# Performance work log

Measured on AMD Instinct MI355X. Metric: run time of the kernel, lower is better.

Reference implementation:

```python
import jax, jax.numpy as jnp
import numpy as np

ALPHA = 0.2  # LeakyReLU negative slope


def setup_inputs() -> dict:
    key = jax.random.key(0)
    k1, k2, k3, k4 = jax.random.split(key, 4)
    N, E, F_IN, F_OUT = 100000, 1600000, 128, 32
    x = jax.random.normal(k1, (N, F_IN), dtype=jnp.float32)
    W = jax.random.normal(k2, (F_IN, F_OUT), dtype=jnp.float32) * 0.1
    a = jax.random.normal(k3, (2 * F_OUT, 1), dtype=jnp.float32) * 0.1
    edge_index = jax.random.randint(k4, (2, E), 0, N, dtype=jnp.int64)
    return {"x": x, "W": W, "a": a, "edge_index": edge_index}


def reference(x, W, a, edge_index):
    N = x.shape[0]
    F_OUT = W.shape[1]
    Wx = x @ W  # [N, F_OUT]
    src = edge_index[0]  # row indices (softmax groups)
    dst = edge_index[1]
    # e = leakyrelu([Wx_i || Wx_j] @ a); split a to avoid materializing the concat
    a_src = a[:F_OUT, 0]
    a_dst = a[F_OUT:, 0]
    e = (Wx @ a_src)[src] + (Wx @ a_dst)[dst]  # [E]
    e = jnp.where(e >= 0, e, ALPHA * e)
    # sparse softmax over rows (src)
    m = jax.ops.segment_max(e, src, num_segments=N)  # -inf for empty rows
    m = jnp.where(jnp.isinf(m), 0.0, m)
    exp_v = jnp.exp(e - m[src])
    s = jax.ops.segment_sum(exp_v, src, num_segments=N)
    s = jnp.where(s == 0, 1.0, s)
    att = exp_v / s[src]  # [E]
    # sparse matmul: h[i] = sum_j att[i,j] * Wx[j]
    h = jax.ops.segment_sum(att[:, None] * Wx[dst], src, num_segments=N)
    return jax.nn.elu(h)
```

## Files before the change

### kernel.cpp

```cpp
#include <hip/hip_runtime.h>
#include <hip/hip_bf16.h>
#include <math.h>

#define ALPHA 0.2f
#define F_IN 128
#define F_OUT 32
#define BSHIFT 7
#define BNODES 128
#define DSTBITS 17
#define CHUNK 8192
#define SLABCAP 3072
#define NBKMAX 800
#define MAXPER 6
#define CURSTRIDE 16

typedef __attribute__((ext_vector_type(8))) short short8;
typedef __attribute__((ext_vector_type(4))) float float4v;

__device__ __forceinline__ short f2bf(float f) {
    __hip_bfloat16 h = __float2bfloat16(f);
    return __builtin_bit_cast(short, h);
}
__device__ __forceinline__ float bf_lo(unsigned u) {
    return __uint_as_float(u << 16);
}
__device__ __forceinline__ float bf_hi(unsigned u) {
    return __uint_as_float(u & 0xFFFF0000u);
}

__global__ __launch_bounds__(512) void k_phaseA(
    const float* __restrict__ x, const float* __restrict__ W,
    const float* __restrict__ a, unsigned short* __restrict__ Wxh,
    float* __restrict__ s1, float* __restrict__ s2, int nTiles, int N, int nT1,
    const int* __restrict__ src, const int* __restrict__ dst,
    int* __restrict__ bcur, unsigned* __restrict__ packed, int E, int NBK)
{
    if ((int)blockIdx.x < nT1) {
        __shared__ short Wt[32 * 136];
        for (int i = threadIdx.x; i < F_IN * F_OUT; i += 512) {
            int k = i >> 5, n = i & 31;
            Wt[n * 136 + k] = f2bf(W[i]);
        }
        __syncthreads();

        int wave = threadIdx.x >> 6;
        int lane = threadIdx.x & 63;
        int tile = blockIdx.x * 8 + wave;
        if (tile >= nTiles) return;

        int m    = lane & 15;
        int quad = lane >> 4;
        int row  = tile * 16 + m;
        int rowc = row < N ? row : N - 1;

        short8 bf[2][4];
#pragma unroll
        for (int t = 0; t < 2; ++t)
#pragma unroll
            for (int s = 0; s < 4; ++s)
                bf[t][s] = *(const short8*)&Wt[(t * 16 + m) * 136 + s * 32 + quad * 8];

        float4v acc0 = {0.f, 0.f, 0.f, 0.f};
        float4v acc1 = {0.f, 0.f, 0.f, 0.f};
        const float* xr = x + (size_t)rowc * F_IN + quad * 8;
#pragma unroll
        for (int s = 0; s < 4; ++s) {
            float4 xa = *(const float4*)(xr + s * 32);
            float4 xb = *(const float4*)(xr + s * 32 + 4);
            short8 af;
            af[0] = f2bf(xa.x); af[1] = f2bf(xa.y); af[2] = f2bf(xa.z); af[3] = f2bf(xa.w);
            af[4] = f2bf(xb.x); af[5] = f2bf(xb.y); af[6] = f2bf(xb.z); af[7] = f2bf(xb.w);
            acc0 = __builtin_amdgcn_mfma_f32_16x16x32_bf16(af, bf[0][s], acc0, 0, 0, 0);
            acc1 = __builtin_amdgcn_mfma_f32_16x16x32_bf16(af, bf[1][s], acc1, 0, 0, 0);
        }

        int rbase = tile * 16 + quad * 4;
#pragma unroll
        for (int r = 0; r < 4; ++r) {
            if (rbase + r < N) {
                Wxh[(size_t)(rbase + r) * F_OUT + m]      = (unsigned short)f2bf(acc0[r]);
                Wxh[(size_t)(rbase + r) * F_OUT + m + 16] = (unsigned short)f2bf(acc1[r]);
            }
        }

        float a1c0 = a[m], a1c1 = a[m + 16];
        float a2c0 = a[F_OUT + m], a2c1 = a[F_OUT + m + 16];
#pragma unroll
        for (int r = 0; r < 4; ++r) {
            float v1 = acc0[r] * a1c0 + acc1[r] * a1c1;
            float v2 = acc0[r] * a2c0 + acc1[r] * a2c1;
#pragma unroll
            for (int off = 8; off >= 1; off >>= 1) {
                v1 += __shfl_xor(v1, off, 16);
                v2 += __shfl_xor(v2, off, 16);
            }
            if (m == 0 && rbase + r < N) {
                s1[rbase + r] = v1;
                s2[rbase + r] = v2;
            }
        }
    } else {
        __shared__ int hist[NBKMAX];
        __shared__ int cur[NBKMAX];
        int t = threadIdx.x;
        for (int i = t; i < NBK; i += 512) hist[i] = 0;
        __syncthreads();
        int e0 = ((int)blockIdx.x - nT1) * CHUNK;
        int sreg[16], dreg[16];
#pragma unroll
        for (int k = 0; k < 4; ++k) {
            int e = e0 + k * 2048 + t * 4;
            int4 s4, d4;
            if (e + 3 < E) {
                s4 = *(const int4*)&src[e];
                d4 = *(const int4*)&dst[e];
            } else {
                s4.x = (e + 0 < E) ? src[e + 0] : -1;
                s4.y = (e + 1 < E) ? src[e + 1] : -1;
                s4.z = (e + 2 < E) ? src[e + 2] : -1;
                s4.w = (e + 3 < E) ? src[e + 3] : -1;
                d4.x = (e + 0 < E) ? dst[e + 0] : 0;
                d4.y = (e + 1 < E) ? dst[e + 1] : 0;
                d4.z = (e + 2 < E) ? dst[e + 2] : 0;
                d4.w = (e + 3 < E) ? dst[e + 3] : 0;
            }
            sreg[k * 4 + 0] = s4.x; dreg[k * 4 + 0] = d4.x;
            sreg[k * 4 + 1] = s4.y; dreg[k * 4 + 1] = d4.y;
            sreg[k * 4 + 2] = s4.z; dreg[k * 4 + 2] = d4.z;
            sreg[k * 4 + 3] = s4.w; dreg[k * 4 + 3] = d4.w;
        }
#pragma unroll
        for (int k = 0; k < 16; ++k)
            if (sreg[k] >= 0) atomicAdd(&hist[sreg[k] >> BSHIFT], 1);
        __syncthreads();
        for (int i = t; i < NBK; i += 512)
            if (hist[i] > 0) cur[i] = atomicAdd(&bcur[i * CURSTRIDE], hist[i]);
        __syncthreads();
#pragma unroll
        for (int k = 0; k < 16; ++k) {
            if (sreg[k] >= 0) {
                int b = sreg[k] >> BSHIFT;
                int p = atomicAdd(&cur[b], 1);
                if (p < SLABCAP)
                    packed[(size_t)b * SLABCAP + p] =
                        ((unsigned)(sreg[k] & (BNODES - 1)) << DSTBITS) | (unsigned)dreg[k];
            }
        }
    }
}

__global__ __launch_bounds__(512) void k_bnode(
    const unsigned* __restrict__ packed, const int* __restrict__ bcur,
    const float* __restrict__ s1, const float* __restrict__ s2,
    const unsigned short* __restrict__ Wxh, float* __restrict__ out, int N)
{
    __shared__ unsigned sorted[SLABCAP];
    __shared__ int rpl[BNODES];
    __shared__ int degl[BNODES];
    __shared__ int cur[BNODES];
    __shared__ int histl[BNODES];
    __shared__ float s1l[BNODES];
    __shared__ float stageL[16][8][32];
    __shared__ float sumsL[16][8];

    int b = blockIdx.x;
    int t = threadIdx.x;
    int n0 = b << BSHIFT;
    int cnt = min(bcur[b * CURSTRIDE], SLABCAP);
    const unsigned* pb = packed + (size_t)b * SLABCAP;

    if (t < BNODES) {
        histl[t] = 0;
        int n = n0 + t;
        s1l[t] = (n < N) ? s1[n] : 0.f;
    }
    __syncthreads();

    unsigned ereg[MAXPER];
#pragma unroll
    for (int k = 0; k < MAXPER; ++k) {
        int j = k * 512 + t;
        ereg[k] = (j < cnt) ? pb[j] : 0xFFFFFFFFu;
    }
#pragma unroll
    for (int k = 0; k < MAXPER; ++k)
        if (ereg[k] != 0xFFFFFFFFu) atomicAdd(&histl[ereg[k] >> DSTBITS], 1);
    __syncthreads();

    if (t < 64) {
        int aLo = histl[t], aHi = histl[t + 64];
        int sLo = aLo, sHi = aHi;
#pragma unroll
        for (int off = 1; off < 64; off <<= 1) {
            int vLo = __shfl_up(sLo, off, 64);
            int vHi = __shfl_up(sHi, off, 64);
            if (t >= off) { sLo += vLo; sHi += vHi; }
        }
        sHi += __shfl(sLo, 63, 64);
        rpl[t]      = sLo - aLo;  cur[t]      = sLo - aLo;  degl[t]      = aLo;
        rpl[t + 64] = sHi - aHi;  cur[t + 64] = sHi - aHi;  degl[t + 64] = aHi;
    }
    __syncthreads();

#pragma unroll
    for (int k = 0; k < MAXPER; ++k) {
        if (ereg[k] != 0xFFFFFFFFu) {
            int ls = ereg[k] >> DSTBITS;
            int p = atomicAdd(&cur[ls], 1);
            sorted[p] = ereg[k];
        }
    }
    __syncthreads();

    int g = t >> 5;
    int l = t & 31;
    int es = l >> 3;
    int fq = l & 7;

    for (int ni = 0; ni < 8; ++ni) {
        int ls = (g << 3) + ni;
        int n = n0 + ls;
        if (n >= N) break;
        int base = rpl[ls];
        int deg  = degl[ls];
        float s1n = s1l[ls];

        float acc[4];
#pragma unroll
        for (int c = 0; c < 4; ++c) acc[c] = 0.f;
        float sum = 0.f;

        for (int j0 = 0; j0 < deg; j0 += 32) {
            int j = j0 + l;
            int   d_l = 0;
            float p_l = 0.f;
            if (j < deg) {
                d_l = (int)(sorted[base + j] & ((1u << DSTBITS) - 1));
                float ev = s1n + s2[d_l];
                ev = ev >= 0.f ? ev : ALPHA * ev;
                p_l = __expf(ev);
            }
            sum += p_l;
            int cnt2 = min(32, deg - j0);
            int nIter = (cnt2 + 3) >> 2;
            for (int it = 0; it < nIter; ++it) {
                int e = (it << 2) + es;
                float p = __shfl(p_l, e, 32);
                int   d = __shfl(d_l, e, 32);
                uint2 w = *(const uint2*)&Wxh[(size_t)d * F_OUT + fq * 4];
                acc[0] += p * bf_lo(w.x);
                acc[1] += p * bf_hi(w.x);
                acc[2] += p * bf_lo(w.y);
                acc[3] += p * bf_hi(w.y);
            }
        }
#pragma unroll
        for (int off = 8; off <= 16; off <<= 1)
#pragma unroll
            for (int c = 0; c < 4; ++c)
                acc[c] += __shfl_xor(acc[c], off, 32);
#pragma unroll
        for (int off = 16; off >= 1; off >>= 1)
            sum += __shfl_xor(sum, off, 32);

        if (l < 8) {
            float4 v;
            v.x = acc[0]; v.y = acc[1]; v.z = acc[2]; v.w = acc[3];
            *(float4*)&stageL[g][ni][l * 4] = v;
        }
        if (l == 0)
            sumsL[g][ni] = sum;
    }

    {
        int ln = l >> 2;
        int fo = (l & 3) * 8;
        int n = n0 + (g << 3) + ln;
        if (n < N) {
            float s = sumsL[g][ln];
            float inv = (s > 0.f) ? __builtin_amdgcn_rcpf(s) : 0.f;
            const float* sp = &stageL[g][ln][fo];
            float4 h0 = *(const float4*)sp;
            float4 h1 = *(const float4*)(sp + 4);
            h0.x *= inv; h0.y *= inv; h0.z *= inv; h0.w *= inv;
            h1.x *= inv; h1.y *= inv; h1.z *= inv; h1.w *= inv;
            h0.x = h0.x > 0.f ? h0.x : __expf(h0.x) - 1.f;
            h0.y = h0.y > 0.f ? h0.y : __expf(h0.y) - 1.f;
            h0.z = h0.z > 0.f ? h0.z : __expf(h0.z) - 1.f;
            h0.w = h0.w > 0.f ? h0.w : __expf(h0.w) - 1.f;
            h1.x = h1.x > 0.f ? h1.x : __expf(h1.x) - 1.f;
            h1.y = h1.y > 0.f ? h1.y : __expf(h1.y) - 1.f;
            h1.z = h1.z > 0.f ? h1.z : __expf(h1.z) - 1.f;
            h1.w = h1.w > 0.f ? h1.w : __expf(h1.w) - 1.f;
            float* op = &out[(size_t)n * F_OUT + fo];
            *(float4*)op       = h0;
            *(float4*)(op + 4) = h1;
        }
    }
}

extern "C" void kernel_launch(void* const* d_in, const int* in_sizes, int n_in,
                              void* d_out, int out_size, void* d_ws, size_t ws_size,
                              hipStream_t stream)
{
    const float* x = (const float*)d_in[0];
    const float* W = (const float*)d_in[1];
    const float* a = (const float*)d_in[2];
    const int*  ei = (const int*)d_in[3];

    int N = in_sizes[0] / F_IN;
    int E = in_sizes[3] / 2;
    const int* src = ei;
    const int* dst = ei + E;
    int NBK = (N + BNODES - 1) >> BSHIFT;
    int nTiles = (N + 15) / 16;
    int nT1 = (nTiles + 7) / 8;
    int nEB = (E + CHUNK - 1) / CHUNK;

    unsigned short* Wxh = (unsigned short*)d_ws;
    float*    s1       = (float*)d_ws + (size_t)16 * N;
    float*    s2       = s1 + N;
    int*      bcur     = (int*)(s2 + N);
    unsigned* packed   = (unsigned*)(bcur + NBKMAX * CURSTRIDE);

    float* out = (float*)d_out;

    hipMemsetAsync(bcur, 0, (size_t)NBKMAX * CURSTRIDE * 4, stream);

    k_phaseA<<<nT1 + nEB, 512, 0, stream>>>(x, W, a, Wxh, s1, s2, nTiles, N, nT1,
                                            src, dst, bcur, packed, E, NBK);
    k_bnode<<<NBK, 512, 0, stream>>>(packed, bcur, s1, s2, Wxh, out, N);
}
```

Baseline: 149.1 us.

## Fuse both phases into one cooperative persistent kernel with grid sync

Replaces the memset plus two kernel launches with a single cooperative kernel. It zeroes the counters itself, runs phase A (GEMM tiles and edge bucketing) and the per-bucket aggregation as persistent loops driven by atomic work counters, and separates the two phases with grid.sync(). Shared memory for the phases is overlaid in a union. This removes launch gaps and the memset, at the cost of grid-sync overhead, an extra atomic fetch per work item, and an occupancy limit on grid size.

```diff
diff --git a/kernel.cpp b/kernel.cpp
--- a/kernel.cpp
+++ b/kernel.cpp
@@ -1,6 +1,9 @@
 #include <hip/hip_runtime.h>
+#include <hip/hip_cooperative_groups.h>
 #include <hip/hip_bf16.h>
 #include <math.h>
+
+namespace cg = cooperative_groups;
 
 #define ALPHA 0.2f
 #define F_IN 128
@@ -28,273 +31,302 @@
     return __uint_as_float(u & 0xFFFF0000u);
 }
 
-__global__ __launch_bounds__(512) void k_phaseA(
+struct SmemGemm { short Wt[32 * 136]; };
+struct SmemBkt  { int hist[NBKMAX]; int cur[NBKMAX]; };
+struct SmemNode {
+    unsigned sorted[SLABCAP];
+    int rpl[BNODES]; int degl[BNODES]; int cur[BNODES]; int histl[BNODES];
+    float s1l[BNODES];
+    float stage[16][8][32];
+    float sums[16][8];
+};
+union SmemU { SmemGemm g; SmemBkt b; SmemNode n; };
+
+__global__ __launch_bounds__(512) void k_fused(
     const float* __restrict__ x, const float* __restrict__ W,
     const float* __restrict__ a, unsigned short* __restrict__ Wxh,
     float* __restrict__ s1, float* __restrict__ s2, int nTiles, int N, int nT1,
     const int* __restrict__ src, const int* __restrict__ dst,
-    int* __restrict__ bcur, unsigned* __restrict__ packed, int E, int NBK)
+    int* __restrict__ bcur, unsigned* __restrict__ packed, int E, int NBK,
+    int nWorkA, float* __restrict__ out)
 {
-    if ((int)blockIdx.x < nT1) {
-        __shared__ short Wt[32 * 136];
-        for (int i = threadIdx.x; i < F_IN * F_OUT; i += 512) {
-            int k = i >> 5, n = i & 31;
-            Wt[n * 136 + k] = f2bf(W[i]);
-        }
-        __syncthreads();
-
-        int wave = threadIdx.x >> 6;
-        int lane = threadIdx.x & 63;
-        int tile = blockIdx.x * 8 + wave;
-        if (tile >= nTiles) return;
-
-        int m    = lane & 15;
-        int quad = lane >> 4;
-        int row  = tile * 16 + m;
-        int rowc = row < N ? row : N - 1;
-
-        short8 bf[2][4];
-#pragma unroll
-        for (int t = 0; t < 2; ++t)
-#pragma unroll
-            for (int s = 0; s < 4; ++s)
-                bf[t][s] = *(const short8*)&Wt[(t * 16 + m) * 136 + s * 32 + quad * 8];
-
-        float4v acc0 = {0.f, 0.f, 0.f, 0.f};
-        float4v acc1 = {0.f, 0.f, 0.f, 0.f};
-        const float* xr = x + (size_t)rowc * F_IN + quad * 8;
-#pragma unroll
-        for (int s = 0; s < 4; ++s) {
-            float4 xa = *(const float4*)(xr + s * 32);
-            float4 xb = *(const float4*)(xr + s * 32 + 4);
-            short8 af;
-            af[0] = f2bf(xa.x); af[1] = f2bf(xa.y); af[2] = f2bf(xa.z); af[3] = f2bf(xa.w);
-            af[4] = f2bf(xb.x); af[5] = f2bf(xb.y); af[6] = f2bf(xb.z); af[7] = f2bf(xb.w);
-            acc0 = __builtin_amdgcn_mfma_f32_16x16x32_bf16(af, bf[0][s], acc0, 0, 0, 0);
-            acc1 = __builtin_amdgcn_mfma_f32_16x16x32_bf16(af, bf[1][s], acc1, 0, 0, 0);
-        }
-
-        int rbase = tile * 16 + quad * 4;
-#pragma unroll
-        for (int r = 0; r < 4; ++r) {
-            if (rbase + r < N) {
-                Wxh[(size_t)(rbase + r) * F_OUT + m]      = (unsigned short)f2bf(acc0[r]);
-                Wxh[(size_t)(rbase + r) * F_OUT + m + 16] = (unsigned short)f2bf(acc1[r]);
-            }
-        }
-
-        float a1c0 = a[m], a1c1 = a[m + 16];
-        float a2c0 = a[F_OUT + m], a2c1 = a[F_OUT + m + 16];
-#pragma unroll
-        for (int r = 0; r < 4; ++r) {
-            float v1 = acc0[r] * a1c0 + acc1[r] * a1c1;
-            float v2 = acc0[r] * a2c0 + acc1[r] * a2c1;
-#pragma unroll
-            for (int off = 8; off >= 1; off >>= 1) {
-                v1 += __shfl_xor(v1, off, 16);
-                v2 += __shfl_xor(v2, off, 16);
-            }
-            if (m == 0 && rbase + r < N) {
-                s1[rbase + r] = v1;
-                s2[rbase + r] = v2;
-            }
-        }
-    } else {
-        __shared__ int hist[NBKMAX];
-        __shared__ int cur[NBKMAX];
-        int t = threadIdx.x;
-        for (int i = t; i < NBK; i += 512) hist[i] = 0;
-        __syncthreads();
-        int e0 = ((int)blockIdx.x - nT1) * CHUNK;
-        int sreg[16], dreg[16];
-#pragma unroll
-        for (int k = 0; k < 4; ++k) {
-            int e = e0 + k * 2048 + t * 4;
-            int4 s4, d4;
-            if (e + 3 < E) {
-                s4 = *(const int4*)&src[e];
-                d4 = *(const int4*)&dst[e];
-            } else {
-                s4.x = (e + 0 < E) ? src[e + 0] : -1;
-                s4.y = (e + 1 < E) ? src[e + 1] : -1;
-                s4.z = (e + 2 < E) ? src[e + 2] : -1;
-                s4.w = (e + 3 < E) ? src[e + 3] : -1;
-                d4.x = (e + 0 < E) ? dst[e + 0] : 0;
-                d4.y = (e + 1 < E) ? dst[e + 1] : 0;
-                d4.z = (e + 2 < E) ? dst[e + 2] : 0;
-                d4.w = (e + 3 < E) ? dst[e + 3] : 0;
-            }
-            sreg[k * 4 + 0] = s4.x; dreg[k * 4 + 0] = d4.x;
-            sreg[k * 4 + 1] = s4.y; dreg[k * 4 + 1] = d4.y;
-            sreg[k * 4 + 2] = s4.z; dreg[k * 4 + 2] = d4.z;
-            sreg[k * 4 + 3] = s4.w; dreg[k * 4 + 3] = d4.w;
-        }
-#pragma unroll
-        for (int k = 0; k < 16; ++k)
-            if (sreg[k] >= 0) atomicAdd(&hist[sreg[k] >> BSHIFT], 1);
-        __syncthreads();
-        for (int i = t; i < NBK; i += 512)
-            if (hist[i] > 0) cur[i] = atomicAdd(&bcur[i * CURSTRIDE], hist[i]);
-        __syncthreads();
-#pragma unroll
-        for (int k = 0; k < 16; ++k) {
-            if (sreg[k] >= 0) {
-                int b = sreg[k] >> BSHIFT;
-                int p = atomicAdd(&cur[b], 1);
-                if (p < SLABCAP)
-                    packed[(size_t)b * SLABCAP + p] =
-                        ((unsigned)(sreg[k] & (BNODES - 1)) << DSTBITS) | (unsigned)dreg[k];
+    cg::grid_group grid = cg::this_grid();
+    __shared__ __align__(16) SmemU sm;
+    __shared__ int witem;
+    int t = threadIdx.x;
+
+    int* ctr = bcur + NBKMAX * CURSTRIDE;
+    for (int i = (int)blockIdx.x * 512 + t; i < NBKMAX * CURSTRIDE + 2 * CURSTRIDE;
+         i += (int)gridDim.x * 512)
+        bcur[i] = 0;
+    grid.sync();
+
+    for (;;) {
+        __syncthreads();
+        if (t == 0) witem = atomicAdd(&ctr[0], 1);
+        __syncthreads();
+        int w = witem;
+        if (w >= nWorkA) break;
+
+        if (w < nT1) {
+            short* Wt = sm.g.Wt;
+            for (int i = t; i < F_IN * F_OUT; i += 512) {
+                int k = i >> 5, n = i & 31;
+                Wt[n * 136 + k] = f2bf(W[i]);
+            }
+            __syncthreads();
+
+            int wave = t >> 6;
+            int lane = t & 63;
+            int tile = w * 8 + wave;
+            if (tile < nTiles) {
+                int m    = lane & 15;
+                int quad = lane >> 4;
+                int row  = tile * 16 + m;
+                int rowc = row < N ? row : N - 1;
+
+                short8 bfr[2][4];
+#pragma unroll
+                for (int tt = 0; tt < 2; ++tt)
+#pragma unroll
+                    for (int s = 0; s < 4; ++s)
+                        bfr[tt][s] = *(const short8*)&Wt[(tt * 16 + m) * 136 + s * 32 + quad * 8];
+
+                float4v acc0 = {0.f, 0.f, 0.f, 0.f};
+                float4v acc1 = {0.f, 0.f, 0.f, 0.f};
+                const float* xr = x + (size_t)rowc * F_IN + quad * 8;
+#pragma unroll
+                for (int s = 0; s < 4; ++s) {
+                    float4 xa = *(const float4*)(xr + s * 32);
+                    float4 xb = *(const float4*)(xr + s * 32 + 4);
+                    short8 af;
+                    af[0] = f2bf(xa.x); af[1] = f2bf(xa.y); af[2] = f2bf(xa.z); af[3] = f2bf(xa.w);
+                    af[4] = f2bf(xb.x); af[5] = f2bf(xb.y); af[6] = f2bf(xb.z); af[7] = f2bf(xb.w);
+                    acc0 = __builtin_amdgcn_mfma_f32_16x16x32_bf16(af, bfr[0][s], acc0, 0, 0, 0);
+                    acc1 = __builtin_amdgcn_mfma_f32_16x16x32_bf16(af, bfr[1][s], acc1, 0, 0, 0);
+                }
+
+                int rbase = tile * 16 + quad * 4;
+#pragma unroll
+                for (int r = 0; r < 4; ++r) {
+                    if (rbase + r < N) {
+                        Wxh[(size_t)(rbase + r) * F_OUT + m]      = (unsigned short)f2bf(acc0[r]);
+                        Wxh[(size_t)(rbase + r) * F_OUT + m + 16] = (unsigned short)f2bf(acc1[r]);
+                    }
+                }
+
+                float a1c0 = a[m], a1c1 = a[m + 16];
+                float a2c0 = a[F_OUT + m], a2c1 = a[F_OUT + m + 16];
+#pragma unroll
+                for (int r = 0; r < 4; ++r) {
+                    float v1 = acc0[r] * a1c0 + acc1[r] * a1c1;
+                    float v2 = acc0[r] * a2c0 + acc1[r] * a2c1;
+#pragma unroll
+                    for (int off = 8; off >= 1; off >>= 1) {
+                        v1 += __shfl_xor(v1, off, 16);
+                        v2 += __shfl_xor(v2, off, 16);
+                    }
+                    if (m == 0 && rbase + r < N) {
+                        s1[rbase + r] = v1;
+                        s2[rbase + r] = v2;
+                    }
+                }
+            }
+        } else {
+            int* hist = sm.b.hist;
+            int* curb = sm.b.cur;
+            for (int i = t; i < NBK; i += 512) hist[i] = 0;
+            __syncthreads();
+            int e0 = (w - nT1) * CHUNK;
+            int sreg[16], dreg[16];
+#pragma unroll
+            for (int k = 0; k < 4; ++k) {
+                int e = e0 + k * 2048 + t * 4;
+                int4 s4, d4;
+                if (e + 3 < E) {
+                    s4 = *(const int4*)&src[e];
+                    d4 = *(const int4*)&dst[e];
+                } else {
+                    s4.x = (e + 0 < E) ? src[e + 0] : -1;
+                    s4.y = (e + 1 < E) ? src[e + 1] : -1;
+                    s4.z = (e + 2 < E) ? src[e + 2] : -1;
+                    s4.w = (e + 3 < E) ? src[e + 3] : -1;
+                    d4.x = (e + 0 < E) ? dst[e + 0] : 0;
+                    d4.y = (e + 1 < E) ? dst[e + 1] : 0;
+                    d4.z = (e + 2 < E) ? dst[e + 2] : 0;
+                    d4.w = (e + 3 < E) ? dst[e + 3] : 0;
+                }
+                sreg[k * 4 + 0] = s4.x; dreg[k * 4 + 0] = d4.x;
+                sreg[k * 4 + 1] = s4.y; dreg[k * 4 + 1] = d4.y;
+                sreg[k * 4 + 2] = s4.z; dreg[k * 4 + 2] = d4.z;
+                sreg[k * 4 + 3] = s4.w; dreg[k * 4 + 3] = d4.w;
+            }
+#pragma unroll
+            for (int k = 0; k < 16; ++k)
+                if (sreg[k] >= 0) atomicAdd(&hist[sreg[k] >> BSHIFT], 1);
+            __syncthreads();
+            for (int i = t; i < NBK; i += 512)
+                if (hist[i] > 0) curb[i] = atomicAdd(&bcur[i * CURSTRIDE], hist[i]);
+            __syncthreads();
+#pragma unroll
+            for (int k = 0; k < 16; ++k) {
+                if (sreg[k] >= 0) {
+                    int b = sreg[k] >> BSHIFT;
+                    int p = atomicAdd(&curb[b], 1);
+                    if (p < SLABCAP)
+                        packed[(size_t)b * SLABCAP + p] =
+                            ((unsigned)(sreg[k] & (BNODES - 1)) << DSTBITS) | (unsigned)dreg[k];
+                }
             }
         }
     }
-}
-
-__global__ __launch_bounds__(512) void k_bnode(
-    const unsigned* __restrict__ packed, const int* __restrict__ bcur,
-    const float* __restrict__ s1, const float* __restrict__ s2,
-    const unsigned short* __restrict__ Wxh, float* __restrict__ out, int N)
-{
-    __shared__ unsigned sorted[SLABCAP];
-    __shared__ int rpl[BNODES];
-    __shared__ int degl[BNODES];
-    __shared__ int cur[BNODES];
-    __shared__ int histl[BNODES];
-    __shared__ float s1l[BNODES];
-    __shared__ float stageL[16][8][32];
-    __shared__ float sumsL[16][8];
-
-    int b = blockIdx.x;
-    int t = threadIdx.x;
-    int n0 = b << BSHIFT;
-    int cnt = min(bcur[b * CURSTRIDE], SLABCAP);
-    const unsigned* pb = packed + (size_t)b * SLABCAP;
-
-    if (t < BNODES) {
-        histl[t] = 0;
-        int n = n0 + t;
-        s1l[t] = (n < N) ? s1[n] : 0.f;
-    }
-    __syncthreads();
-
-    unsigned ereg[MAXPER];
-#pragma unroll
-    for (int k = 0; k < MAXPER; ++k) {
-        int j = k * 512 + t;
-        ereg[k] = (j < cnt) ? pb[j] : 0xFFFFFFFFu;
-    }
-#pragma unroll
-    for (int k = 0; k < MAXPER; ++k)
-        if (ereg[k] != 0xFFFFFFFFu) atomicAdd(&histl[ereg[k] >> DSTBITS], 1);
-    __syncthreads();
-
-    if (t < 64) {
-        int aLo = histl[t], aHi = histl[t + 64];
-        int sLo = aLo, sHi = aHi;
-#pragma unroll
-        for (int off = 1; off < 64; off <<= 1) {
-            int vLo = __shfl_up(sLo, off, 64);
-            int vHi = __shfl_up(sHi, off, 64);
-            if (t >= off) { sLo += vLo; sHi += vHi; }
-        }
-        sHi += __shfl(sLo, 63, 64);
-        rpl[t]      = sLo - aLo;  cur[t]      = sLo - aLo;  degl[t]      = aLo;
-        rpl[t + 64] = sHi - aHi;  cur[t + 64] = sHi - aHi;  degl[t + 64] = aHi;
-    }
-    __syncthreads();
-
-#pragma unroll
-    for (int k = 0; k < MAXPER; ++k) {
-        if (ereg[k] != 0xFFFFFFFFu) {
-            int ls = ereg[k] >> DSTBITS;
-            int p = atomicAdd(&cur[ls], 1);
-            sorted[p] = ereg[k];
-        }
-    }
-    __syncthreads();
-
-    int g = t >> 5;
-    int l = t & 31;
-    int es = l >> 3;
-    int fq = l & 7;
-
-    for (int ni = 0; ni < 8; ++ni) {
-        int ls = (g << 3) + ni;
-        int n = n0 + ls;
-        if (n >= N) break;
-        int base = rpl[ls];
-        int deg  = degl[ls];
-        float s1n = s1l[ls];
-
-        float acc[4];
-#pragma unroll
-        for (int c = 0; c < 4; ++c) acc[c] = 0.f;
-        float sum = 0.f;
-
-        for (int j0 = 0; j0 < deg; j0 += 32) {
-            int j = j0 + l;
-            int   d_l = 0;
-            float p_l = 0.f;
-            if (j < deg) {
-                d_l = (int)(sorted[base + j] & ((1u << DSTBITS) - 1));
-                float ev = s1n + s2[d_l];
-                ev = ev >= 0.f ? ev : ALPHA * ev;
-                p_l = __expf(ev);
-            }
-            sum += p_l;
-            int cnt2 = min(32, deg - j0);
-            int nIter = (cnt2 + 3) >> 2;
-            for (int it = 0; it < nIter; ++it) {
-                int e = (it << 2) + es;
-                float p = __shfl(p_l, e, 32);
-                int   d = __shfl(d_l, e, 32);
-                uint2 w = *(const uint2*)&Wxh[(size_t)d * F_OUT + fq * 4];
-                acc[0] += p * bf_lo(w.x);
-                acc[1] += p * bf_hi(w.x);
-                acc[2] += p * bf_lo(w.y);
-                acc[3] += p * bf_hi(w.y);
-            }
-        }
-#pragma unroll
-        for (int off = 8; off <= 16; off <<= 1)
-#pragma unroll
-            for (int c = 0; c < 4; ++c)
-                acc[c] += __shfl_xor(acc[c], off, 32);
-#pragma unroll
-        for (int off = 16; off >= 1; off >>= 1)
-            sum += __shfl_xor(sum, off, 32);
-
-        if (l < 8) {
-            float4 v;
-            v.x = acc[0]; v.y = acc[1]; v.z = acc[2]; v.w = acc[3];
-            *(float4*)&stageL[g][ni][l * 4] = v;
-        }
-        if (l == 0)
-            sumsL[g][ni] = sum;
-    }
-
-    {
-        int ln = l >> 2;
-        int fo = (l & 3) * 8;
-        int n = n0 + (g << 3) + ln;
-        if (n < N) {
-            float s = sumsL[g][ln];
-            float inv = (s > 0.f) ? __builtin_amdgcn_rcpf(s) : 0.f;
-            const float* sp = &stageL[g][ln][fo];
-            float4 h0 = *(const float4*)sp;
-            float4 h1 = *(const float4*)(sp + 4);
-            h0.x *= inv; h0.y *= inv; h0.z *= inv; h0.w *= inv;
-            h1.x *= inv; h1.y *= inv; h1.z *= inv; h1.w *= inv;
-            h0.x = h0.x > 0.f ? h0.x : __expf(h0.x) - 1.f;
-            h0.y = h0.y > 0.f ? h0.y : __expf(h0.y) - 1.f;
-            h0.z = h0.z > 0.f ? h0.z : __expf(h0.z) - 1.f;
-            h0.w = h0.w > 0.f ? h0.w : __expf(h0.w) - 1.f;
-            h1.x = h1.x > 0.f ? h1.x : __expf(h1.x) - 1.f;
-            h1.y = h1.y > 0.f ? h1.y : __expf(h1.y) - 1.f;
-            h1.z = h1.z > 0.f ? h1.z : __expf(h1.z) - 1.f;
-            h1.w = h1.w > 0.f ? h1.w : __expf(h1.w) - 1.f;
-            float* op = &out[(size_t)n * F_OUT + fo];
-            *(float4*)op       = h0;
-            *(float4*)(op + 4) = h1;
+    grid.sync();
+
+    for (;;) {
+        __syncthreads();
+        if (t == 0) witem = atomicAdd(&ctr[CURSTRIDE], 1);
+        __syncthreads();
+        int b = witem;
+        if (b >= NBK) break;
+
+        unsigned* sorted = sm.n.sorted;
+        int* rpl   = sm.n.rpl;
+        int* degl  = sm.n.degl;
+        int* curn  = sm.n.cur;
+        int* histl = sm.n.histl;
+        float* s1l = sm.n.s1l;
+
+        int n0 = b << BSHIFT;
+        int cnt = min(bcur[b * CURSTRIDE], SLABCAP);
+        const unsigned* pb = packed + (size_t)b * SLABCAP;
+
+        if (t < BNODES) {
+            histl[t] = 0;
+            int n = n0 + t;
+            s1l[t] = (n < N) ? s1[n] : 0.f;
+        }
+        __syncthreads();
+
+        unsigned ereg[MAXPER];
+#pragma unroll
+        for (int k = 0; k < MAXPER; ++k) {
+            int j = k * 512 + t;
+            ereg[k] = (j < cnt) ? pb[j] : 0xFFFFFFFFu;
+        }
+#pragma unroll
+        for (int k = 0; k < MAXPER; ++k)
+            if (ereg[k] != 0xFFFFFFFFu) atomicAdd(&histl[ereg[k] >> DSTBITS], 1);
+        __syncthreads();
+
+        if (t < 64) {
+            int aLo = histl[t], aHi = histl[t + 64];
+            int sLo = aLo, sHi = aHi;
+#pragma unroll
+            for (int off = 1; off < 64; off <<= 1) {
+                int vLo = __shfl_up(sLo, off, 64);
+                int vHi = __shfl_up(sHi, off, 64);
+                if (t >= off) { sLo += vLo; sHi += vHi; }
+            }
+            sHi += __shfl(sLo, 63, 64);
+            rpl[t]      = sLo - aLo;  curn[t]      = sLo - aLo;  degl[t]      = aLo;
+            rpl[t + 64] = sHi - aHi;  curn[t + 64] = sHi - aHi;  degl[t + 64] = aHi;
+        }
+        __syncthreads();
+
+#pragma unroll
+        for (int k = 0; k < MAXPER; ++k) {
+            if (ereg[k] != 0xFFFFFFFFu) {
+                int ls = ereg[k] >> DSTBITS;
+                int p = atomicAdd(&curn[ls], 1);
+                sorted[p] = ereg[k];
+            }
+        }
+        __syncthreads();
+
+        int g = t >> 5;
+        int l = t & 31;
+        int es = l >> 3;
+        int fq = l & 7;
+
+        for (int ni = 0; ni < 8; ++ni) {
+            int ls = (g << 3) + ni;
+            int n = n0 + ls;
+            if (n >= N) break;
+            int base = rpl[ls];
+            int deg  = degl[ls];
+            float s1n = s1l[ls];
+
+            float acc[4];
+#pragma unroll
+            for (int c = 0; c < 4; ++c) acc[c] = 0.f;
+            float sum = 0.f;
+
+            for (int j0 = 0; j0 < deg; j0 += 32) {
+                int j = j0 + l;
+                int   d_l = 0;
+                float p_l = 0.f;
+                if (j < deg) {
+                    d_l = (int)(sorted[base + j] & ((1u << DSTBITS) - 1));
+                    float ev = s1n + s2[d_l];
+                    ev = ev >= 0.f ? ev : ALPHA * ev;
+                    p_l = __expf(ev);
+                }
+                sum += p_l;
+                int cnt2 = min(32, deg - j0);
+                int nIter = (cnt2 + 3) >> 2;
+                for (int it = 0; it < nIter; ++it) {
+                    int e = (it << 2) + es;
+                    float p = __shfl(p_l, e, 32);
+                    int   d = __shfl(d_l, e, 32);
+                    uint2 wv = *(const uint2*)&Wxh[(size_t)d * F_OUT + fq * 4];
+                    acc[0] += p * bf_lo(wv.x);
+                    acc[1] += p * bf_hi(wv.x);
+                    acc[2] += p * bf_lo(wv.y);
+                    acc[3] += p * bf_hi(wv.y);
+                }
+            }
+#pragma unroll
+            for (int off = 8; off <= 16; off <<= 1)
+#pragma unroll
+                for (int c = 0; c < 4; ++c)
+                    acc[c] += __shfl_xor(acc[c], off, 32);
+#pragma unroll
+            for (int off = 16; off >= 1; off >>= 1)
+                sum += __shfl_xor(sum, off, 32);
+
+            if (l < 8) {
+                float4 v;
+                v.x = acc[0]; v.y = acc[1]; v.z = acc[2]; v.w = acc[3];
+                *(float4*)&sm.n.stage[g][ni][l * 4] = v;
+            }
+            if (l == 0)
+                sm.n.sums[g][ni] = sum;
+        }
+
+        {
+            int ln = l >> 2;
+            int fo = (l & 3) * 8;
+            int n = n0 + (g << 3) + ln;
+            if (n < N) {
+                float s = sm.n.sums[g][ln];
+                float inv = (s > 0.f) ? __builtin_amdgcn_rcpf(s) : 0.f;
+                const float* sp = &sm.n.stage[g][ln][fo];
+                float4 h0 = *(const float4*)sp;
+                float4 h1 = *(const float4*)(sp + 4);
+                h0.x *= inv; h0.y *= inv; h0.z *= inv; h0.w *= inv;
+                h1.x *= inv; h1.y *= inv; h1.z *= inv; h1.w *= inv;
+                h0.x = h0.x > 0.f ? h0.x : __expf(h0.x) - 1.f;
+                h0.y = h0.y > 0.f ? h0.y : __expf(h0.y) - 1.f;
+                h0.z = h0.z > 0.f ? h0.z : __expf(h0.z) - 1.f;
+                h0.w = h0.w > 0.f ? h0.w : __expf(h0.w) - 1.f;
+                h1.x = h1.x > 0.f ? h1.x : __expf(h1.x) - 1.f;
+                h1.y = h1.y > 0.f ? h1.y : __expf(h1.y) - 1.f;
+                h1.z = h1.z > 0.f ? h1.z : __expf(h1.z) - 1.f;
+                h1.w = h1.w > 0.f ? h1.w : __expf(h1.w) - 1.f;
+                float* op = &out[(size_t)n * F_OUT + fo];
+                *(float4*)op       = h0;
+                *(float4*)(op + 4) = h1;
+            }
         }
     }
 }
@@ -316,18 +348,34 @@
     int nTiles = (N + 15) / 16;
     int nT1 = (nTiles + 7) / 8;
     int nEB = (E + CHUNK - 1) / CHUNK;
+    int nWorkA = nT1 + nEB;
 
     unsigned short* Wxh = (unsigned short*)d_ws;
     float*    s1       = (float*)d_ws + (size_t)16 * N;
     float*    s2       = s1 + N;
     int*      bcur     = (int*)(s2 + N);
-    unsigned* packed   = (unsigned*)(bcur + NBKMAX * CURSTRIDE);
+    unsigned* packed   = (unsigned*)(bcur + NBKMAX * CURSTRIDE + 2 * CURSTRIDE);
 
     float* out = (float*)d_out;
 
-    hipMemsetAsync(bcur, 0, (size_t)NBKMAX * CURSTRIDE * 4, stream);
-
-    k_phaseA<<<nT1 + nEB, 512, 0, stream>>>(x, W, a, Wxh, s1, s2, nTiles, N, nT1,
-                                            src, dst, bcur, packed, E, NBK);
-    k_bnode<<<NBK, 512, 0, stream>>>(packed, bcur, s1, s2, Wxh, out, N);
-}
+    static int s_maxco = 0;
+    if (s_maxco == 0) {
+        int nb = 0;
+        hipOccupancyMaxActiveBlocksPerMultiprocessor(&nb, k_fused, 512, 0);
+        if (nb < 1) nb = 1;
+        int dev = 0, cu = 0;
+        hipGetDevice(&dev);
+        hipDeviceGetAttribute(&cu, hipDeviceAttributeMultiprocessorCount, dev);
+        if (cu <= 0) cu = 256;
+        s_maxco = nb * cu;
+    }
+    int maxWork = nWorkA > NBK ? nWorkA : NBK;
+    int grid = s_maxco < maxWork ? s_maxco : maxWork;
+
+    void* args[] = {(void*)&x, (void*)&W, (void*)&a, (void*)&Wxh, (void*)&s1,
+                    (void*)&s2, (void*)&nTiles, (void*)&N, (void*)&nT1,
+                    (void*)&src, (void*)&dst, (void*)&bcur, (void*)&packed,
+                    (void*)&E, (void*)&NBK, (void*)&nWorkA, (void*)&out};
+    hipLaunchCooperativeKernel((const void*)k_fused, dim3(grid), dim3(512),
+                               args, 0, stream);
+}
```

Measured after the change: 277.4 us. +86.0%, slower.
